# Performance work log

Hardware: AMD Instinct MI355X
Metric: run time of the kernel (lower is better)

## Reference

```python
import jax, jax.numpy as jnp
import numpy as np

NUM_EXPERTS = 8
TOP_K = 2


def setup_inputs() -> dict:
    key = jax.random.key(0)
    k1, k2, k3, k4 = jax.random.split(key, 4)
    B, T, C, E, D = 4, 2048, 2048, NUM_EXPERTS, 2048
    scale = 0.02
    return {
        "x": jax.random.normal(k1, (B, T, C), dtype=jnp.float32),
        "w_router": jax.random.normal(k2, (C, E), dtype=jnp.float32) * scale,
        "w_fc": jax.random.normal(k3, (E, C, D), dtype=jnp.float32) * scale,
        "w_proj": jax.random.normal(k4, (E, D, C), dtype=jnp.float32) * scale,
    }


def reference(x, w_router, w_fc, w_proj):
    B, T, C = x.shape
    E = w_fc.shape[0]
    x_flat = x.reshape(-1, C)                       # [N, C]
    N = x_flat.shape[0]

    router_logits = x_flat @ w_router                # [N, E]
    top_vals, top_idx = jax.lax.top_k(router_logits, TOP_K)  # [N, K]
    probs = jax.nn.softmax(top_vals, axis=-1)        # [N, K]

    # Per-token combine weight for each expert (0 if not selected).
    rows = jnp.arange(N)[:, None]                    # [N, 1]
    w_tok = jnp.zeros((N, E), dtype=x.dtype).at[rows, top_idx].add(probs)  # [N, E]

    # Dense grouped computation over experts (same math as masked loop):
    # hidden = relu(x W_fc)^2, then project and combine with routing weights.
    h = jnp.einsum('nc,ecd->ned', x_flat, w_fc)      # [N, E, D]
    h = jnp.square(jax.nn.relu(h))
    y = jnp.einsum('ned,edc->nec', h, w_proj)        # [N, E, C]
    out = jnp.einsum('nec,ne->nc', y, w_tok)         # [N, C]
    return out.reshape(B, T, C)
```

## Files before the change

kernel.cpp:

```cpp
#include <hip/hip_runtime.h>

typedef float   f32x4 __attribute__((ext_vector_type(4)));
typedef _Float16 f16x8 __attribute__((ext_vector_type(8)));
typedef short   s16x8 __attribute__((ext_vector_type(8)));
typedef short   s16x4 __attribute__((ext_vector_type(4)));
typedef unsigned short u16;

#define NTOK 8192
#define CDIM 2048
#define NEXP 8
#define NASS 16384
#define MTILES 24

#define GLOBAL_AS __attribute__((address_space(1)))
#define LDS_AS    __attribute__((address_space(3)))

__device__ __forceinline__ u16 f2h_bits(float f) {
  _Float16 h = (_Float16)f;
  union { _Float16 h; u16 u; } v;
  v.h = h;
  return v.u;
}

__global__ __launch_bounds__(256) void moe_wrt(
    const float* __restrict__ wr, float* __restrict__ wrT)
{
  const int gid = blockIdx.x * 256 + threadIdx.x;
  const int c = gid >> 3, e = gid & 7;
  wrT[e * CDIM + c] = wr[c * NEXP + e];
}

__global__ __launch_bounds__(256) void moe_router(
    const float* __restrict__ x, const float* __restrict__ wrT,
    u16* __restrict__ xh, int* __restrict__ top_idx,
    float* __restrict__ top_p, int* __restrict__ counts)
{
  __shared__ int scnt[NEXP];
  if (threadIdx.x < NEXP) scnt[threadIdx.x] = 0;
  __syncthreads();
  const int wave = threadIdx.x >> 6, lane = threadIdx.x & 63;
  for (int i = 0; i < 8; ++i) {
    const int n = blockIdx.x * 32 + i * 4 + wave;
    const float* xr = x + (size_t)n * CDIM;
    u16* xhr = xh + (size_t)n * CDIM;
    float acc[NEXP] = {};
    #pragma unroll
    for (int ii = 0; ii < CDIM / 256; ++ii) {
      const int c = ii * 256 + lane * 4;
      const f32x4 xv = *(const f32x4*)(xr + c);
      s16x4 hv;
      #pragma unroll
      for (int j = 0; j < 4; ++j) hv[j] = (short)f2h_bits(xv[j]);
      *(s16x4*)(xhr + c) = hv;
      #pragma unroll
      for (int e = 0; e < NEXP; ++e) {
        const f32x4 wv = *(const f32x4*)(wrT + (size_t)e * CDIM + c);
        acc[e] += xv[0]*wv[0] + xv[1]*wv[1] + xv[2]*wv[2] + xv[3]*wv[3];
      }
    }
    #pragma unroll
    for (int off = 32; off > 0; off >>= 1) {
      #pragma unroll
      for (int e = 0; e < NEXP; ++e) acc[e] += __shfl_xor(acc[e], off);
    }
    if (lane == 0) {
      int i0 = 0; float v0 = acc[0];
      #pragma unroll
      for (int e = 1; e < NEXP; ++e) { if (acc[e] > v0) { v0 = acc[e]; i0 = e; } }
      int i1 = -1; float v1 = -3.4e38f;
      #pragma unroll
      for (int e = 0; e < NEXP; ++e) { if (e != i0 && acc[e] > v1) { v1 = acc[e]; i1 = e; } }
      const float ex = __expf(v1 - v0);
      const float p0 = 1.f / (1.f + ex);
      top_idx[n * 2 + 0] = i0; top_idx[n * 2 + 1] = i1;
      top_p[n * 2 + 0] = p0;   top_p[n * 2 + 1] = 1.f - p0;
      atomicAdd(&scnt[i0], 1);
      atomicAdd(&scnt[i1], 1);
    }
  }
  __syncthreads();
  if (threadIdx.x < NEXP) atomicAdd(&counts[threadIdx.x], scnt[threadIdx.x]);
}

__global__ void moe_offsets(const int* __restrict__ counts,
                            int* __restrict__ offs, int* __restrict__ fill)
{
  if (threadIdx.x == 0) {
    int s = 0;
    for (int e = 0; e < NEXP; ++e) { offs[e] = s; fill[e] = s; s += counts[e]; }
    offs[NEXP] = s;
  }
}

__global__ __launch_bounds__(256) void moe_scatter(
    const int* __restrict__ top_idx, const float* __restrict__ top_p,
    int* fill, int* __restrict__ tok_s, float* __restrict__ prb_s)
{
  const int n = blockIdx.x * 256 + threadIdx.x;
  #pragma unroll
  for (int k = 0; k < 2; ++k) {
    const int e = top_idx[n * 2 + k];
    const int pos = atomicAdd(&fill[e], 1);
    tok_s[pos] = n;
    prb_s[pos] = top_p[n * 2 + k];
  }
}

__global__ __launch_bounds__(256) void moe_transpose(
    const float* __restrict__ wfc, const float* __restrict__ wpj,
    u16* __restrict__ wfcT, u16* __restrict__ wpjT)
{
  const float* src = blockIdx.z ? wpj : wfc;
  u16* dst = blockIdx.z ? wpjT : wfcT;
  const int e = blockIdx.y;
  src += (size_t)e * CDIM * CDIM;
  dst += (size_t)e * CDIM * CDIM;
  const int tr = (blockIdx.x >> 4) * 64;
  const int tc = (blockIdx.x & 15) * 128;
  __shared__ float lds[64][129];
  const int t = threadIdx.x;
  #pragma unroll
  for (int p = 0; p < 8; ++p) {
    const int r  = p * 8 + (t >> 5);
    const int c4 = (t & 31) * 4;
    const f32x4 v = *(const f32x4*)(src + (size_t)(tr + r) * CDIM + tc + c4);
    #pragma unroll
    for (int j = 0; j < 4; ++j) lds[r][c4 + j] = v[j];
  }
  __syncthreads();
  const int d  = t >> 1;
  const int ks = (t & 1) * 32;
  u16* drow = dst + (size_t)(tc + d) * CDIM + tr + ks;
  #pragma unroll
  for (int q = 0; q < 4; ++q) {
    s16x8 o;
    #pragma unroll
    for (int j = 0; j < 8; ++j) o[j] = (short)f2h_bits(lds[ks + q * 8 + j][d]);
    *(s16x8*)(drow + q * 8) = o;
  }
}

template<int MODE>
__global__ __launch_bounds__(512, 4) void moe_gemm9(
    const u16* __restrict__ A, const u16* __restrict__ W,
    const int* __restrict__ tok_s, const float* __restrict__ prb_s,
    const int* __restrict__ offs, u16* __restrict__ hout,
    float* __restrict__ out)
{
  const int id    = blockIdx.x;
  const int nt    = id & 7;
  const int rid   = id >> 3;
  const int e     = rid / MTILES;
  const int mtile = rid % MTILES;
  const int off0  = offs[e];
  const int Me    = offs[e + 1] - off0;
  const int m0    = mtile * 128;
  if (m0 >= Me) return;
  const int n0 = nt * 256;
  const u16* We = W + (size_t)e * CDIM * CDIM;

  __shared__ u16 As[3][128 * 32];
  __shared__ u16 Bs[3][256 * 32];

  const int t    = threadIdx.x;
  const int lane = t & 63, wv = t >> 6;
  const int wm = wv >> 2, wn = wv & 3;

  const int l     = lane;
  const int kchnk = (l & 3) ^ ((l >> 3) & 3);
  const int kelem = kchnk * 8;
  const int rloc  = 2 * (l >> 3) + ((l >> 2) & 1);
  const int rA  = wv * 16 + rloc;
  const int mrA = m0 + rA;
  const int rrA = (mrA < Me) ? mrA : (Me - 1);
  const int gaA = (MODE == 0) ? tok_s[off0 + rrA] : (off0 + rrA);
  const u16* asrc = A + (size_t)gaA * CDIM + kelem;
  const int rB0 = wv * 32 + rloc;
  const int rB1 = wv * 32 + 16 + rloc;
  const u16* bsrc0 = We + (size_t)(n0 + rB0) * CDIM + kelem;
  const u16* bsrc1 = We + (size_t)(n0 + rB1) * CDIM + kelem;

  #define STAGE(T_, bb_)                                                       \
    { const int kk_ = (T_) * 32;                                               \
      __builtin_amdgcn_global_load_lds(                                        \
          (const GLOBAL_AS void*)(asrc + kk_),                                 \
          (LDS_AS void*)&As[bb_][wv * 512], 16, 0, 0);                         \
      __builtin_amdgcn_global_load_lds(                                        \
          (const GLOBAL_AS void*)(bsrc0 + kk_),                                \
          (LDS_AS void*)&Bs[bb_][wv * 1024], 16, 0, 0);                        \
      __builtin_amdgcn_global_load_lds(                                        \
          (const GLOBAL_AS void*)(bsrc1 + kk_),                                \
          (LDS_AS void*)&Bs[bb_][wv * 1024 + 512], 16, 0, 0); }

  const int rsel     = lane & 15;
  const int g        = lane >> 4;
  const int halfline = rsel >> 1;
  const int slotx    = (((rsel & 1) * 4) + (g ^ (halfline & 3))) * 8;

  f32x4 acc[4][4] = {};

  #define COMPUTE(bb)                                                          \
    { f16x8 bv[4];                                                             \
      _Pragma("unroll")                                                        \
      for (int fn = 0; fn < 4; ++fn)                                           \
        bv[fn] = *(const f16x8*)&Bs[bb][(wn * 32 + fn * 8 + halfline) * 64 + slotx]; \
      _Pragma("unroll")                                                        \
      for (int fi = 0; fi < 4; ++fi) {                                         \
        const f16x8 av = *(const f16x8*)&As[bb][(wm * 32 + fi * 8 + halfline) * 64 + slotx]; \
        _Pragma("unroll")                                                      \
        for (int fn = 0; fn < 4; ++fn)                                         \
          acc[fi][fn] = __builtin_amdgcn_mfma_f32_16x16x32_f16(                \
              av, bv[fn], acc[fi][fn], 0, 0, 0);                               \
      } }

  STAGE(0, 0); STAGE(1, 1);
  int bb = 0;
  #pragma unroll 3
  for (int T = 0; T < 64; ++T) {
    if (T < 63) { asm volatile("s_waitcnt vmcnt(3)" ::: "memory"); }
    else        { asm volatile("s_waitcnt vmcnt(0)" ::: "memory"); }
    __builtin_amdgcn_s_barrier();
    if (T < 62) {
      const int b2 = (bb >= 1) ? bb - 1 : bb + 2;
      STAGE(T + 2, b2);
    }
    COMPUTE(bb);
    bb = (bb == 2) ? 0 : bb + 1;
  }
  #undef STAGE
  #undef COMPUTE

  const int crow = g * 4;
  const int ccol = rsel;
  #pragma unroll
  for (int fi = 0; fi < 4; ++fi) {
    #pragma unroll
    for (int j = 0; j < 4; ++j) {
      const int r = m0 + wm * 64 + fi * 16 + crow + j;
      if (r >= Me) continue;
      const int s = off0 + r;
      if (MODE == 0) {
        u16* hr = hout + (size_t)s * CDIM;
        #pragma unroll
        for (int fn = 0; fn < 4; ++fn) {
          float v = acc[fi][fn][j];
          v = v > 0.f ? v * v : 0.f;
          hr[n0 + wn * 64 + fn * 16 + ccol] = f2h_bits(v);
        }
      } else {
        const float p = prb_s[s];
        float* orow = out + (size_t)tok_s[s] * CDIM;
        #pragma unroll
        for (int fn = 0; fn < 4; ++fn)
          atomicAdd(&orow[n0 + wn * 64 + fn * 16 + ccol], p * acc[fi][fn][j]);
      }
    }
  }
}

extern "C" void kernel_launch(void* const* d_in, const int* in_sizes, int n_in,
                              void* d_out, int out_size, void* d_ws, size_t ws_size,
                              hipStream_t stream)
{
  const float* x   = (const float*)d_in[0];
  const float* wr  = (const float*)d_in[1];
  const float* wfc = (const float*)d_in[2];
  const float* wpj = (const float*)d_in[3];
  float* out = (float*)d_out;
  char* ws = (char*)d_ws;

  const size_t OFF_TIDX = 256;
  const size_t OFF_TP   = OFF_TIDX + (size_t)NASS * 4;
  const size_t OFF_TOK  = OFF_TP   + (size_t)NASS * 4;
  const size_t OFF_PRB  = OFF_TOK  + (size_t)NASS * 4;
  const size_t OFF_WRT  = OFF_PRB  + (size_t)NASS * 4;
  const size_t OFF_XH   = (size_t)1 << 20;
  const size_t OFF_WFCT = OFF_XH   + (size_t)NTOK * CDIM * 2;
  const size_t OFF_WPJT = OFF_WFCT + (size_t)NEXP * CDIM * CDIM * 2;
  const size_t OFF_H    = OFF_WPJT + (size_t)NEXP * CDIM * CDIM * 2;
  const size_t NEED     = OFF_H    + (size_t)NASS * CDIM * 2;

  if (ws_size < NEED) {
    hipMemsetAsync(d_out, 0, (size_t)out_size * 4, stream);
    return;
  }

  int*   counts = (int*)(ws + 0);
  int*   offs   = (int*)(ws + 64);
  int*   fill   = (int*)(ws + 128);
  int*   tidx   = (int*)(ws + OFF_TIDX);
  float* tp     = (float*)(ws + OFF_TP);
  int*   tok    = (int*)(ws + OFF_TOK);
  float* prb    = (float*)(ws + OFF_PRB);
  float* wrT    = (float*)(ws + OFF_WRT);
  u16*   xh     = (u16*)(ws + OFF_XH);
  u16*   wfcT   = (u16*)(ws + OFF_WFCT);
  u16*   wpjT   = (u16*)(ws + OFF_WPJT);
  u16*   h      = (u16*)(ws + OFF_H);

  hipMemsetAsync(ws, 0, 256, stream);
  hipMemsetAsync(d_out, 0, (size_t)out_size * 4, stream);

  moe_wrt     <<<NEXP * CDIM / 256, 256, 0, stream>>>(wr, wrT);
  moe_router  <<<256, 256, 0, stream>>>(x, wrT, xh, tidx, tp, counts);
  moe_offsets <<<1, 64, 0, stream>>>(counts, offs, fill);
  moe_scatter <<<NTOK / 256, 256, 0, stream>>>(tidx, tp, fill, tok, prb);
  moe_transpose<<<dim3(512, NEXP, 2), 256, 0, stream>>>(wfc, wpj, wfcT, wpjT);
  moe_gemm9<0><<<NEXP * 8 * MTILES, 512, 0, stream>>>(xh, wfcT, tok, nullptr, offs, h, nullptr);
  moe_gemm9<1><<<NEXP * 8 * MTILES, 512, 0, stream>>>(h,  wpjT, tok, prb,     offs, nullptr, out);
}
```

Baseline: 610.8 us.

## Enlarge MoE GEMM tile to 256x256 with split-phase pipelined LDS staging

Doubles the M tile of the grouped expert GEMM from 128 to 256 rows, so each block keeps 8x4 accumulator fragments per wave and reuses each loaded weight tile across twice as many tokens. The main loop is split into two half-phases that interleave A/B global-to-LDS staging with the MFMA blocks, and uses s_setprio around the MFMA bursts. Launch bounds drop to 2 blocks per CU to fit the larger register and LDS footprint. The aim is to cut weight-reload traffic and improve overlap, at the cost of lower occupancy and more tail waste when an expert's row count is not a multiple of 256.

```diff
diff --git a/kernel.cpp b/kernel.cpp
--- a/kernel.cpp
+++ b/kernel.cpp
@@ -10,7 +10,7 @@
 #define CDIM 2048
 #define NEXP 8
 #define NASS 16384
-#define MTILES 24
+#define MT10 12
 
 #define GLOBAL_AS __attribute__((address_space(1)))
 #define LDS_AS    __attribute__((address_space(3)))
@@ -141,7 +141,7 @@
 }
 
 template<int MODE>
-__global__ __launch_bounds__(512, 4) void moe_gemm9(
+__global__ __launch_bounds__(512, 2) void moe_gemm10(
     const u16* __restrict__ A, const u16* __restrict__ W,
     const int* __restrict__ tok_s, const float* __restrict__ prb_s,
     const int* __restrict__ offs, u16* __restrict__ hout,
@@ -150,16 +150,16 @@
   const int id    = blockIdx.x;
   const int nt    = id & 7;
   const int rid   = id >> 3;
-  const int e     = rid / MTILES;
-  const int mtile = rid % MTILES;
+  const int e     = rid / MT10;
+  const int mtile = rid % MT10;
   const int off0  = offs[e];
   const int Me    = offs[e + 1] - off0;
-  const int m0    = mtile * 128;
+  const int m0    = mtile * 256;
   if (m0 >= Me) return;
   const int n0 = nt * 256;
   const u16* We = W + (size_t)e * CDIM * CDIM;
 
-  __shared__ u16 As[3][128 * 32];
+  __shared__ u16 As[3][256 * 32];
   __shared__ u16 Bs[3][256 * 32];
 
   const int t    = threadIdx.x;
@@ -170,73 +170,91 @@
   const int kchnk = (l & 3) ^ ((l >> 3) & 3);
   const int kelem = kchnk * 8;
   const int rloc  = 2 * (l >> 3) + ((l >> 2) & 1);
-  const int rA  = wv * 16 + rloc;
-  const int mrA = m0 + rA;
-  const int rrA = (mrA < Me) ? mrA : (Me - 1);
-  const int gaA = (MODE == 0) ? tok_s[off0 + rrA] : (off0 + rrA);
-  const u16* asrc = A + (size_t)gaA * CDIM + kelem;
-  const int rB0 = wv * 32 + rloc;
-  const int rB1 = wv * 32 + 16 + rloc;
-  const u16* bsrc0 = We + (size_t)(n0 + rB0) * CDIM + kelem;
-  const u16* bsrc1 = We + (size_t)(n0 + rB1) * CDIM + kelem;
-
-  #define STAGE(T_, bb_)                                                       \
+  const int rA0 = wv * 32 + rloc;
+  const int rA1 = wv * 32 + 16 + rloc;
+  int mr0 = m0 + rA0; mr0 = mr0 < Me ? mr0 : Me - 1;
+  int mr1 = m0 + rA1; mr1 = mr1 < Me ? mr1 : Me - 1;
+  const int ga0 = (MODE == 0) ? tok_s[off0 + mr0] : (off0 + mr0);
+  const int ga1 = (MODE == 0) ? tok_s[off0 + mr1] : (off0 + mr1);
+  const u16* asrc0 = A  + (size_t)ga0 * CDIM + kelem;
+  const u16* asrc1 = A  + (size_t)ga1 * CDIM + kelem;
+  const u16* bsrc0 = We + (size_t)(n0 + rA0) * CDIM + kelem;
+  const u16* bsrc1 = We + (size_t)(n0 + rA1) * CDIM + kelem;
+  const int dA0 = wv * 1024;
+  const int dA1 = wv * 1024 + 512;
+
+  #define STG_A(bb_, T_)                                                       \
     { const int kk_ = (T_) * 32;                                               \
-      __builtin_amdgcn_global_load_lds(                                        \
-          (const GLOBAL_AS void*)(asrc + kk_),                                 \
-          (LDS_AS void*)&As[bb_][wv * 512], 16, 0, 0);                         \
-      __builtin_amdgcn_global_load_lds(                                        \
-          (const GLOBAL_AS void*)(bsrc0 + kk_),                                \
-          (LDS_AS void*)&Bs[bb_][wv * 1024], 16, 0, 0);                        \
-      __builtin_amdgcn_global_load_lds(                                        \
-          (const GLOBAL_AS void*)(bsrc1 + kk_),                                \
-          (LDS_AS void*)&Bs[bb_][wv * 1024 + 512], 16, 0, 0); }
+      __builtin_amdgcn_global_load_lds((const GLOBAL_AS void*)(asrc0 + kk_),   \
+          (LDS_AS void*)&As[bb_][dA0], 16, 0, 0);                              \
+      __builtin_amdgcn_global_load_lds((const GLOBAL_AS void*)(asrc1 + kk_),   \
+          (LDS_AS void*)&As[bb_][dA1], 16, 0, 0); }
+  #define STG_B(bb_, T_)                                                       \
+    { const int kk_ = (T_) * 32;                                               \
+      __builtin_amdgcn_global_load_lds((const GLOBAL_AS void*)(bsrc0 + kk_),   \
+          (LDS_AS void*)&Bs[bb_][dA0], 16, 0, 0);                              \
+      __builtin_amdgcn_global_load_lds((const GLOBAL_AS void*)(bsrc1 + kk_),   \
+          (LDS_AS void*)&Bs[bb_][dA1], 16, 0, 0); }
 
   const int rsel     = lane & 15;
   const int g        = lane >> 4;
   const int halfline = rsel >> 1;
   const int slotx    = (((rsel & 1) * 4) + (g ^ (halfline & 3))) * 8;
 
-  f32x4 acc[4][4] = {};
-
-  #define COMPUTE(bb)                                                          \
-    { f16x8 bv[4];                                                             \
+  f32x4 acc[8][4] = {};
+  f16x8 av[4], bv[4];
+
+  #define READ_B(bb) { _Pragma("unroll")                                       \
+    for (int fn = 0; fn < 4; ++fn)                                             \
+      bv[fn] = *(const f16x8*)&Bs[bb][(wn * 32 + fn * 8 + halfline) * 64 + slotx]; }
+  #define READ_A(bb, mh) { _Pragma("unroll")                                   \
+    for (int fi = 0; fi < 4; ++fi)                                             \
+      av[fi] = *(const f16x8*)&As[bb][(wm * 64 + (mh) * 32 + fi * 8 + halfline) * 64 + slotx]; }
+  #define MFMA16(mh) { _Pragma("unroll")                                       \
+    for (int fi = 0; fi < 4; ++fi)                                             \
       _Pragma("unroll")                                                        \
       for (int fn = 0; fn < 4; ++fn)                                           \
-        bv[fn] = *(const f16x8*)&Bs[bb][(wn * 32 + fn * 8 + halfline) * 64 + slotx]; \
-      _Pragma("unroll")                                                        \
-      for (int fi = 0; fi < 4; ++fi) {                                         \
-        const f16x8 av = *(const f16x8*)&As[bb][(wm * 32 + fi * 8 + halfline) * 64 + slotx]; \
-        _Pragma("unroll")                                                      \
-        for (int fn = 0; fn < 4; ++fn)                                         \
-          acc[fi][fn] = __builtin_amdgcn_mfma_f32_16x16x32_f16(                \
-              av, bv[fn], acc[fi][fn], 0, 0, 0);                               \
-      } }
-
-  STAGE(0, 0); STAGE(1, 1);
-  int bb = 0;
-  #pragma unroll 3
+        acc[(mh) * 4 + fi][fn] = __builtin_amdgcn_mfma_f32_16x16x32_f16(       \
+            av[fi], bv[fn], acc[(mh) * 4 + fi][fn], 0, 0, 0); }
+
+  STG_A(0, 0); STG_B(0, 0); STG_A(1, 1); STG_B(1, 1);
+  asm volatile("s_waitcnt vmcnt(4)" ::: "memory");
+  __builtin_amdgcn_s_barrier();
+
+  int b0 = 0, b1 = 1, b2 = 2;
   for (int T = 0; T < 64; ++T) {
-    if (T < 63) { asm volatile("s_waitcnt vmcnt(3)" ::: "memory"); }
-    else        { asm volatile("s_waitcnt vmcnt(0)" ::: "memory"); }
+    READ_B(b0);
+    READ_A(b0, 0);
+    if (T < 62) STG_A(b2, T + 2);
     __builtin_amdgcn_s_barrier();
-    if (T < 62) {
-      const int b2 = (bb >= 1) ? bb - 1 : bb + 2;
-      STAGE(T + 2, b2);
-    }
-    COMPUTE(bb);
-    bb = (bb == 2) ? 0 : bb + 1;
-  }
-  #undef STAGE
-  #undef COMPUTE
+    asm volatile("s_waitcnt lgkmcnt(0)" ::: "memory");
+    __builtin_amdgcn_s_setprio(1);
+    MFMA16(0);
+    __builtin_amdgcn_s_setprio(0);
+    READ_A(b0, 1);
+    if (T < 62) STG_B(b2, T + 2);
+    if (T < 62)       { asm volatile("s_waitcnt vmcnt(4)" ::: "memory"); }
+    else if (T == 62) { asm volatile("s_waitcnt vmcnt(0)" ::: "memory"); }
+    __builtin_amdgcn_s_barrier();
+    asm volatile("s_waitcnt lgkmcnt(0)" ::: "memory");
+    __builtin_amdgcn_s_setprio(1);
+    MFMA16(1);
+    __builtin_amdgcn_s_setprio(0);
+    const int tmp = b0; b0 = b1; b1 = b2; b2 = tmp;
+  }
+  #undef STG_A
+  #undef STG_B
+  #undef READ_A
+  #undef READ_B
+  #undef MFMA16
 
   const int crow = g * 4;
   const int ccol = rsel;
   #pragma unroll
-  for (int fi = 0; fi < 4; ++fi) {
+  for (int fi = 0; fi < 8; ++fi) {
     #pragma unroll
     for (int j = 0; j < 4; ++j) {
-      const int r = m0 + wm * 64 + fi * 16 + crow + j;
+      const int r = m0 + wm * 128 + fi * 16 + crow + j;
       if (r >= Me) continue;
       const int s = off0 + r;
       if (MODE == 0) {
@@ -306,6 +324,6 @@
   moe_offsets <<<1, 64, 0, stream>>>(counts, offs, fill);
   moe_scatter <<<NTOK / 256, 256, 0, stream>>>(tidx, tp, fill, tok, prb);
   moe_transpose<<<dim3(512, NEXP, 2), 256, 0, stream>>>(wfc, wpj, wfcT, wpjT);
-  moe_gemm9<0><<<NEXP * 8 * MTILES, 512, 0, stream>>>(xh, wfcT, tok, nullptr, offs, h, nullptr);
-  moe_gemm9<1><<<NEXP * 8 * MTILES, 512, 0, stream>>>(h,  wpjT, tok, prb,     offs, nullptr, out);
-}
+  moe_gemm10<0><<<NEXP * 8 * MT10, 512, 0, stream>>>(xh, wfcT, tok, nullptr, offs, h, nullptr);
+  moe_gemm10<1><<<NEXP * 8 * MT10, 512, 0, stream>>>(h,  wpjT, tok, prb,     offs, nullptr, out);
+}
```

Measured after the change: 683.1 us. 11.8% more time.

## Fuse router with weight transpose and merge both expert GEMMs into persistent kernel

Applied to the files above, without the earlier changes.

Merges the router and weight-transpose kernels into one launch, and replaces the two grouped GEMM launches with a single persistent 512-block kernel. That kernel walks the up-projection tiles first, then the down-projection tiles, and waits on per-expert completion counters so down-projection work on finished experts can start while other experts are still in the first GEMM. The K-loop pipeline also changes to prefetch three stages ahead with an extra barrier per iteration. The goal is to remove launch gaps and tail idle time between phases. In exchange the kernel spin-waits across blocks, the M-tile cap per expert drops from 24 to 20, and the added barrier could slow the inner loop.

```diff
diff --git a/kernel.cpp b/kernel.cpp
--- a/kernel.cpp
+++ b/kernel.cpp
@@ -10,7 +10,9 @@
 #define CDIM 2048
 #define NEXP 8
 #define NASS 16384
-#define MTILES 24
+#define MT   20
+#define ITEMS_PER_MODE (NEXP * MT * 8)
+#define EXPECTED_PER_E (MT * 8)
 
 #define GLOBAL_AS __attribute__((address_space(1)))
 #define LDS_AS    __attribute__((address_space(3)))
@@ -30,56 +32,93 @@
   wrT[e * CDIM + c] = wr[c * NEXP + e];
 }
 
-__global__ __launch_bounds__(256) void moe_router(
+__global__ __launch_bounds__(256) void moe_prep(
     const float* __restrict__ x, const float* __restrict__ wrT,
     u16* __restrict__ xh, int* __restrict__ top_idx,
-    float* __restrict__ top_p, int* __restrict__ counts)
-{
-  __shared__ int scnt[NEXP];
-  if (threadIdx.x < NEXP) scnt[threadIdx.x] = 0;
-  __syncthreads();
-  const int wave = threadIdx.x >> 6, lane = threadIdx.x & 63;
-  for (int i = 0; i < 8; ++i) {
-    const int n = blockIdx.x * 32 + i * 4 + wave;
-    const float* xr = x + (size_t)n * CDIM;
-    u16* xhr = xh + (size_t)n * CDIM;
-    float acc[NEXP] = {};
+    float* __restrict__ top_p, int* __restrict__ counts,
+    const float* __restrict__ wfc, const float* __restrict__ wpj,
+    u16* __restrict__ wfcT, u16* __restrict__ wpjT)
+{
+  __shared__ __attribute__((aligned(16))) char shm[64 * 129 * 4];
+  const int id = blockIdx.x;
+  if (id < 256) {
+    int* scnt = (int*)shm;
+    if (threadIdx.x < NEXP) scnt[threadIdx.x] = 0;
+    __syncthreads();
+    const int wave = threadIdx.x >> 6, lane = threadIdx.x & 63;
+    for (int i = 0; i < 8; ++i) {
+      const int n = id * 32 + i * 4 + wave;
+      const float* xr = x + (size_t)n * CDIM;
+      u16* xhr = xh + (size_t)n * CDIM;
+      float acc[NEXP] = {};
+      #pragma unroll
+      for (int ii = 0; ii < CDIM / 256; ++ii) {
+        const int c = ii * 256 + lane * 4;
+        const f32x4 xv = *(const f32x4*)(xr + c);
+        s16x4 hv;
+        #pragma unroll
+        for (int j = 0; j < 4; ++j) hv[j] = (short)f2h_bits(xv[j]);
+        *(s16x4*)(xhr + c) = hv;
+        #pragma unroll
+        for (int e = 0; e < NEXP; ++e) {
+          const f32x4 wv = *(const f32x4*)(wrT + (size_t)e * CDIM + c);
+          acc[e] += xv[0]*wv[0] + xv[1]*wv[1] + xv[2]*wv[2] + xv[3]*wv[3];
+        }
+      }
+      #pragma unroll
+      for (int off = 32; off > 0; off >>= 1) {
+        #pragma unroll
+        for (int e = 0; e < NEXP; ++e) acc[e] += __shfl_xor(acc[e], off);
+      }
+      if (lane == 0) {
+        int i0 = 0; float v0 = acc[0];
+        #pragma unroll
+        for (int e = 1; e < NEXP; ++e) { if (acc[e] > v0) { v0 = acc[e]; i0 = e; } }
+        int i1 = -1; float v1 = -3.4e38f;
+        #pragma unroll
+        for (int e = 0; e < NEXP; ++e) { if (e != i0 && acc[e] > v1) { v1 = acc[e]; i1 = e; } }
+        const float ex = __expf(v1 - v0);
+        const float p0 = 1.f / (1.f + ex);
+        top_idx[n * 2 + 0] = i0; top_idx[n * 2 + 1] = i1;
+        top_p[n * 2 + 0] = p0;   top_p[n * 2 + 1] = 1.f - p0;
+        atomicAdd(&scnt[i0], 1);
+        atomicAdd(&scnt[i1], 1);
+      }
+    }
+    __syncthreads();
+    if (threadIdx.x < NEXP) atomicAdd(&counts[threadIdx.x], scnt[threadIdx.x]);
+  } else {
+    float (*lds)[129] = (float(*)[129])shm;
+    const int tid2 = id - 256;
+    const int z  = tid2 >> 12;
+    const int r2 = tid2 & 4095;
+    const int e  = r2 >> 9;
+    const int xb = r2 & 511;
+    const float* src = (z ? wpj : wfc) + (size_t)e * CDIM * CDIM;
+    u16* dst = (z ? wpjT : wfcT) + (size_t)e * CDIM * CDIM;
+    const int tr = (xb >> 4) * 64;
+    const int tc = (xb & 15) * 128;
+    const int t = threadIdx.x;
     #pragma unroll
-    for (int ii = 0; ii < CDIM / 256; ++ii) {
-      const int c = ii * 256 + lane * 4;
-      const f32x4 xv = *(const f32x4*)(xr + c);
-      s16x4 hv;
+    for (int p = 0; p < 8; ++p) {
+      const int r  = p * 8 + (t >> 5);
+      const int c4 = (t & 31) * 4;
+      const f32x4 v = *(const f32x4*)(src + (size_t)(tr + r) * CDIM + tc + c4);
       #pragma unroll
-      for (int j = 0; j < 4; ++j) hv[j] = (short)f2h_bits(xv[j]);
-      *(s16x4*)(xhr + c) = hv;
+      for (int j = 0; j < 4; ++j) lds[r][c4 + j] = v[j];
+    }
+    __syncthreads();
+    const int d  = t >> 1;
+    const int ks = (t & 1) * 32;
+    u16* drow = dst + (size_t)(tc + d) * CDIM + tr + ks;
+    #pragma unroll
+    for (int q = 0; q < 4; ++q) {
+      s16x8 o;
       #pragma unroll
-      for (int e = 0; e < NEXP; ++e) {
-        const f32x4 wv = *(const f32x4*)(wrT + (size_t)e * CDIM + c);
-        acc[e] += xv[0]*wv[0] + xv[1]*wv[1] + xv[2]*wv[2] + xv[3]*wv[3];
-      }
-    }
-    #pragma unroll
-    for (int off = 32; off > 0; off >>= 1) {
-      #pragma unroll
-      for (int e = 0; e < NEXP; ++e) acc[e] += __shfl_xor(acc[e], off);
-    }
-    if (lane == 0) {
-      int i0 = 0; float v0 = acc[0];
-      #pragma unroll
-      for (int e = 1; e < NEXP; ++e) { if (acc[e] > v0) { v0 = acc[e]; i0 = e; } }
-      int i1 = -1; float v1 = -3.4e38f;
-      #pragma unroll
-      for (int e = 0; e < NEXP; ++e) { if (e != i0 && acc[e] > v1) { v1 = acc[e]; i1 = e; } }
-      const float ex = __expf(v1 - v0);
-      const float p0 = 1.f / (1.f + ex);
-      top_idx[n * 2 + 0] = i0; top_idx[n * 2 + 1] = i1;
-      top_p[n * 2 + 0] = p0;   top_p[n * 2 + 1] = 1.f - p0;
-      atomicAdd(&scnt[i0], 1);
-      atomicAdd(&scnt[i1], 1);
-    }
-  }
-  __syncthreads();
-  if (threadIdx.x < NEXP) atomicAdd(&counts[threadIdx.x], scnt[threadIdx.x]);
+      for (int j = 0; j < 8; ++j) o[j] = (short)f2h_bits(lds[ks + q * 8 + j][d]);
+      *(s16x8*)(drow + q * 8) = o;
+    }
+  }
 }
 
 __global__ void moe_offsets(const int* __restrict__ counts,
@@ -106,59 +145,12 @@
   }
 }
 
-__global__ __launch_bounds__(256) void moe_transpose(
-    const float* __restrict__ wfc, const float* __restrict__ wpj,
-    u16* __restrict__ wfcT, u16* __restrict__ wpjT)
-{
-  const float* src = blockIdx.z ? wpj : wfc;
-  u16* dst = blockIdx.z ? wpjT : wfcT;
-  const int e = blockIdx.y;
-  src += (size_t)e * CDIM * CDIM;
-  dst += (size_t)e * CDIM * CDIM;
-  const int tr = (blockIdx.x >> 4) * 64;
-  const int tc = (blockIdx.x & 15) * 128;
-  __shared__ float lds[64][129];
-  const int t = threadIdx.x;
-  #pragma unroll
-  for (int p = 0; p < 8; ++p) {
-    const int r  = p * 8 + (t >> 5);
-    const int c4 = (t & 31) * 4;
-    const f32x4 v = *(const f32x4*)(src + (size_t)(tr + r) * CDIM + tc + c4);
-    #pragma unroll
-    for (int j = 0; j < 4; ++j) lds[r][c4 + j] = v[j];
-  }
-  __syncthreads();
-  const int d  = t >> 1;
-  const int ks = (t & 1) * 32;
-  u16* drow = dst + (size_t)(tc + d) * CDIM + tr + ks;
-  #pragma unroll
-  for (int q = 0; q < 4; ++q) {
-    s16x8 o;
-    #pragma unroll
-    for (int j = 0; j < 8; ++j) o[j] = (short)f2h_bits(lds[ks + q * 8 + j][d]);
-    *(s16x8*)(drow + q * 8) = o;
-  }
-}
-
-template<int MODE>
-__global__ __launch_bounds__(512, 4) void moe_gemm9(
-    const u16* __restrict__ A, const u16* __restrict__ W,
-    const int* __restrict__ tok_s, const float* __restrict__ prb_s,
-    const int* __restrict__ offs, u16* __restrict__ hout,
-    float* __restrict__ out)
-{
-  const int id    = blockIdx.x;
-  const int nt    = id & 7;
-  const int rid   = id >> 3;
-  const int e     = rid / MTILES;
-  const int mtile = rid % MTILES;
-  const int off0  = offs[e];
-  const int Me    = offs[e + 1] - off0;
-  const int m0    = mtile * 128;
-  if (m0 >= Me) return;
-  const int n0 = nt * 256;
-  const u16* We = W + (size_t)e * CDIM * CDIM;
-
+__global__ __launch_bounds__(512, 4) void moe_mega(
+    const u16* __restrict__ xh, const u16* __restrict__ wfcT,
+    const u16* __restrict__ wpjT, const int* __restrict__ tok_s,
+    const float* __restrict__ prb_s, const int* __restrict__ offs,
+    int* __restrict__ done0, u16* __restrict__ h, float* __restrict__ out)
+{
   __shared__ u16 As[3][128 * 32];
   __shared__ u16 Bs[3][256 * 32];
 
@@ -170,90 +162,130 @@
   const int kchnk = (l & 3) ^ ((l >> 3) & 3);
   const int kelem = kchnk * 8;
   const int rloc  = 2 * (l >> 3) + ((l >> 2) & 1);
-  const int rA  = wv * 16 + rloc;
-  const int mrA = m0 + rA;
-  const int rrA = (mrA < Me) ? mrA : (Me - 1);
-  const int gaA = (MODE == 0) ? tok_s[off0 + rrA] : (off0 + rrA);
-  const u16* asrc = A + (size_t)gaA * CDIM + kelem;
-  const int rB0 = wv * 32 + rloc;
-  const int rB1 = wv * 32 + 16 + rloc;
-  const u16* bsrc0 = We + (size_t)(n0 + rB0) * CDIM + kelem;
-  const u16* bsrc1 = We + (size_t)(n0 + rB1) * CDIM + kelem;
-
-  #define STAGE(T_, bb_)                                                       \
-    { const int kk_ = (T_) * 32;                                               \
-      __builtin_amdgcn_global_load_lds(                                        \
-          (const GLOBAL_AS void*)(asrc + kk_),                                 \
-          (LDS_AS void*)&As[bb_][wv * 512], 16, 0, 0);                         \
-      __builtin_amdgcn_global_load_lds(                                        \
-          (const GLOBAL_AS void*)(bsrc0 + kk_),                                \
-          (LDS_AS void*)&Bs[bb_][wv * 1024], 16, 0, 0);                        \
-      __builtin_amdgcn_global_load_lds(                                        \
-          (const GLOBAL_AS void*)(bsrc1 + kk_),                                \
-          (LDS_AS void*)&Bs[bb_][wv * 1024 + 512], 16, 0, 0); }
-
   const int rsel     = lane & 15;
   const int g        = lane >> 4;
   const int halfline = rsel >> 1;
   const int slotx    = (((rsel & 1) * 4) + (g ^ (halfline & 3))) * 8;
-
-  f32x4 acc[4][4] = {};
-
-  #define COMPUTE(bb)                                                          \
-    { f16x8 bv[4];                                                             \
-      _Pragma("unroll")                                                        \
-      for (int fn = 0; fn < 4; ++fn)                                           \
-        bv[fn] = *(const f16x8*)&Bs[bb][(wn * 32 + fn * 8 + halfline) * 64 + slotx]; \
-      _Pragma("unroll")                                                        \
-      for (int fi = 0; fi < 4; ++fi) {                                         \
-        const f16x8 av = *(const f16x8*)&As[bb][(wm * 32 + fi * 8 + halfline) * 64 + slotx]; \
-        _Pragma("unroll")                                                      \
-        for (int fn = 0; fn < 4; ++fn)                                         \
-          acc[fi][fn] = __builtin_amdgcn_mfma_f32_16x16x32_f16(                \
-              av, bv[fn], acc[fi][fn], 0, 0, 0);                               \
-      } }
-
-  STAGE(0, 0); STAGE(1, 1);
-  int bb = 0;
-  #pragma unroll 3
-  for (int T = 0; T < 64; ++T) {
-    if (T < 63) { asm volatile("s_waitcnt vmcnt(3)" ::: "memory"); }
-    else        { asm volatile("s_waitcnt vmcnt(0)" ::: "memory"); }
-    __builtin_amdgcn_s_barrier();
-    if (T < 62) {
-      const int b2 = (bb >= 1) ? bb - 1 : bb + 2;
-      STAGE(T + 2, b2);
-    }
-    COMPUTE(bb);
-    bb = (bb == 2) ? 0 : bb + 1;
-  }
-  #undef STAGE
-  #undef COMPUTE
-
   const int crow = g * 4;
   const int ccol = rsel;
-  #pragma unroll
-  for (int fi = 0; fi < 4; ++fi) {
-    #pragma unroll
-    for (int j = 0; j < 4; ++j) {
-      const int r = m0 + wm * 64 + fi * 16 + crow + j;
-      if (r >= Me) continue;
-      const int s = off0 + r;
-      if (MODE == 0) {
-        u16* hr = hout + (size_t)s * CDIM;
-        #pragma unroll
-        for (int fn = 0; fn < 4; ++fn) {
-          float v = acc[fi][fn][j];
-          v = v > 0.f ? v * v : 0.f;
-          hr[n0 + wn * 64 + fn * 16 + ccol] = f2h_bits(v);
+
+  #pragma unroll 1
+  for (int wid = blockIdx.x; wid < 2 * ITEMS_PER_MODE; wid += 512) {
+    const int mode  = (wid >= ITEMS_PER_MODE);
+    const int i     = mode ? wid - ITEMS_PER_MODE : wid;
+    const int nt    = i & 7;
+    const int rest  = i >> 3;
+    const int e     = rest / MT;
+    const int mtile = rest % MT;
+    const int off0  = offs[e];
+    const int Me    = offs[e + 1] - off0;
+    const int m0    = mtile * 128;
+    const bool alive = (m0 < Me);
+
+    if (mode == 1 && alive) {
+      if (t == 0) {
+        while (__hip_atomic_load(&done0[e], __ATOMIC_ACQUIRE,
+                                 __HIP_MEMORY_SCOPE_AGENT) < EXPECTED_PER_E)
+          __builtin_amdgcn_s_sleep(2);
+      }
+    }
+    __syncthreads();
+
+    if (alive) {
+      const int n0 = nt * 256;
+      const u16* We = (mode ? wpjT : wfcT) + (size_t)e * CDIM * CDIM;
+      const u16* Am = mode ? h : xh;
+
+      const int rA  = wv * 16 + rloc;
+      const int mrA = m0 + rA;
+      const int rrA = (mrA < Me) ? mrA : (Me - 1);
+      const int gaA = mode ? (off0 + rrA) : tok_s[off0 + rrA];
+      const u16* asrc = Am + (size_t)gaA * CDIM + kelem;
+      const int rB0 = wv * 32 + rloc;
+      const int rB1 = wv * 32 + 16 + rloc;
+      const u16* bsrc0 = We + (size_t)(n0 + rB0) * CDIM + kelem;
+      const u16* bsrc1 = We + (size_t)(n0 + rB1) * CDIM + kelem;
+
+      #define STAGE(T_, bb_)                                                   \
+        { const int kk_ = (T_) * 32;                                           \
+          __builtin_amdgcn_global_load_lds(                                    \
+              (const GLOBAL_AS void*)(asrc + kk_),                             \
+              (LDS_AS void*)&As[bb_][wv * 512], 16, 0, 0);                     \
+          __builtin_amdgcn_global_load_lds(                                    \
+              (const GLOBAL_AS void*)(bsrc0 + kk_),                            \
+              (LDS_AS void*)&Bs[bb_][wv * 1024], 16, 0, 0);                    \
+          __builtin_amdgcn_global_load_lds(                                    \
+              (const GLOBAL_AS void*)(bsrc1 + kk_),                            \
+              (LDS_AS void*)&Bs[bb_][wv * 1024 + 512], 16, 0, 0); }
+
+      f32x4 acc[4][4] = {};
+
+      #define COMPUTE(bb)                                                      \
+        { f16x8 bv[4];                                                         \
+          _Pragma("unroll")                                                    \
+          for (int fn = 0; fn < 4; ++fn)                                       \
+            bv[fn] = *(const f16x8*)&Bs[bb][(wn * 32 + fn * 8 + halfline) * 64 + slotx]; \
+          _Pragma("unroll")                                                    \
+          for (int fi = 0; fi < 4; ++fi) {                                     \
+            const f16x8 av = *(const f16x8*)&As[bb][(wm * 32 + fi * 8 + halfline) * 64 + slotx]; \
+            _Pragma("unroll")                                                  \
+            for (int fn = 0; fn < 4; ++fn)                                     \
+              acc[fi][fn] = __builtin_amdgcn_mfma_f32_16x16x32_f16(            \
+                  av, bv[fn], acc[fi][fn], 0, 0, 0);                           \
+          } }
+
+      STAGE(0, 0); STAGE(1, 1); STAGE(2, 2);
+      int bb = 0;
+      #pragma unroll 3
+      for (int T = 0; T < 64; ++T) {
+        if (T < 62)       { asm volatile("s_waitcnt vmcnt(6)" ::: "memory"); }
+        else if (T == 62) { asm volatile("s_waitcnt vmcnt(3)" ::: "memory"); }
+        else              { asm volatile("s_waitcnt vmcnt(0)" ::: "memory"); }
+        __builtin_amdgcn_s_barrier();
+        COMPUTE(bb);
+        __builtin_amdgcn_s_barrier();
+        if (T < 61) STAGE(T + 3, bb);
+        bb = (bb == 2) ? 0 : bb + 1;
+      }
+      #undef STAGE
+      #undef COMPUTE
+
+      if (mode == 0) {
+        #pragma unroll
+        for (int fi = 0; fi < 4; ++fi) {
+          #pragma unroll
+          for (int j = 0; j < 4; ++j) {
+            const int r = m0 + wm * 64 + fi * 16 + crow + j;
+            if (r >= Me) continue;
+            u16* hr = h + (size_t)(off0 + r) * CDIM;
+            #pragma unroll
+            for (int fn = 0; fn < 4; ++fn) {
+              float v = acc[fi][fn][j];
+              v = v > 0.f ? v * v : 0.f;
+              hr[n0 + wn * 64 + fn * 16 + ccol] = f2h_bits(v);
+            }
+          }
         }
+        __syncthreads();
+        if (t == 0) { __threadfence(); atomicAdd(&done0[e], 1); }
       } else {
-        const float p = prb_s[s];
-        float* orow = out + (size_t)tok_s[s] * CDIM;
-        #pragma unroll
-        for (int fn = 0; fn < 4; ++fn)
-          atomicAdd(&orow[n0 + wn * 64 + fn * 16 + ccol], p * acc[fi][fn][j]);
-      }
+        #pragma unroll
+        for (int fi = 0; fi < 4; ++fi) {
+          #pragma unroll
+          for (int j = 0; j < 4; ++j) {
+            const int r = m0 + wm * 64 + fi * 16 + crow + j;
+            if (r >= Me) continue;
+            const int s = off0 + r;
+            const float p = prb_s[s];
+            float* orow = out + (size_t)tok_s[s] * CDIM;
+            #pragma unroll
+            for (int fn = 0; fn < 4; ++fn)
+              atomicAdd(&orow[n0 + wn * 64 + fn * 16 + ccol], p * acc[fi][fn][j]);
+          }
+        }
+      }
+    } else if (mode == 0) {
+      if (t == 0) atomicAdd(&done0[e], 1);
     }
   }
 }
@@ -288,6 +320,7 @@
   int*   counts = (int*)(ws + 0);
   int*   offs   = (int*)(ws + 64);
   int*   fill   = (int*)(ws + 128);
+  int*   done0  = (int*)(ws + 192);
   int*   tidx   = (int*)(ws + OFF_TIDX);
   float* tp     = (float*)(ws + OFF_TP);
   int*   tok    = (int*)(ws + OFF_TOK);
@@ -301,11 +334,11 @@
   hipMemsetAsync(ws, 0, 256, stream);
   hipMemsetAsync(d_out, 0, (size_t)out_size * 4, stream);
 
-  moe_wrt     <<<NEXP * CDIM / 256, 256, 0, stream>>>(wr, wrT);
-  moe_router  <<<256, 256, 0, stream>>>(x, wrT, xh, tidx, tp, counts);
+  moe_wrt     <<<64, 256, 0, stream>>>(wr, wrT);
+  moe_prep    <<<256 + 8192, 256, 0, stream>>>(x, wrT, xh, tidx, tp, counts,
+                                               wfc, wpj, wfcT, wpjT);
   moe_offsets <<<1, 64, 0, stream>>>(counts, offs, fill);
   moe_scatter <<<NTOK / 256, 256, 0, stream>>>(tidx, tp, fill, tok, prb);
-  moe_transpose<<<dim3(512, NEXP, 2), 256, 0, stream>>>(wfc, wpj, wfcT, wpjT);
-  moe_gemm9<0><<<NEXP * 8 * MTILES, 512, 0, stream>>>(xh, wfcT, tok, nullptr, offs, h, nullptr);
-  moe_gemm9<1><<<NEXP * 8 * MTILES, 512, 0, stream>>>(h,  wpjT, tok, prb,     offs, nullptr, out);
-}
+  moe_mega    <<<512, 512, 0, stream>>>(xh, wfcT, wpjT, tok, prb, offs,
+                                        done0, h, out);
+}
```

After: 690.2 us. 13.0% more time.
